# Kernel tuning notes

Hardware: AMD Instinct MI355X
Metric: run time of the kernel (lower is better)

Reference implementation:

```python
import jax, jax.numpy as jnp
import numpy as np

ALPHA = 1.5      # entmax alpha (q parameter)
N_ITER = 50      # entmax-bisect iterations (entmax library default)
B, S, DM, H, HKV, HD = 1, 2048, 2048, 16, 4, 128
ROPE_THETA = 10000.0


def _entmax_p(x):
    """alpha-entmax along last axis via bisection on tau (matches entmax.EntmaxBisect)."""
    am1 = ALPHA - 1.0
    pw = 1.0 / am1
    X = x * am1
    d = x.shape[-1]
    max_val = jnp.max(X, axis=-1, keepdims=True)
    tau_lo = max_val - 1.0                      # _gp(1, alpha) = 1
    tau_hi = max_val - (1.0 / d) ** am1          # _gp(1/d, alpha)
    dm0 = tau_hi - tau_lo

    def body(i, carry):
        tau_lo, dm, tau_m = carry
        dm = dm * 0.5
        tau_m = tau_lo + dm
        p = jnp.maximum(X - tau_m, 0.0) ** pw
        f = jnp.sum(p, axis=-1, keepdims=True) - 1.0
        tau_lo = jnp.where(f >= 0, tau_m, tau_lo)
        return (tau_lo, dm, tau_m)

    tau_lo, dm, tau_m = jax.lax.fori_loop(0, N_ITER, body, (tau_lo, dm0, tau_lo))
    p = jnp.maximum(X - tau_m, 0.0) ** pw
    return p / jnp.sum(p, axis=-1, keepdims=True)  # ensure_sum_one


@jax.custom_vjp
def entmax_bisect(x):
    return _entmax_p(x)

def _emx_fwd(x):
    p = _entmax_p(x)
    return p, p

def _emx_bwd(p, g):
    # entmax library backward: gppr = p^(2-alpha) on support
    gppr = jnp.where(p > 0, p ** (2.0 - ALPHA), 0.0)
    dX = g * gppr
    q = jnp.sum(dX, axis=-1, keepdims=True) / jnp.sum(gppr, axis=-1, keepdims=True)
    return ((dX - q * gppr),)

entmax_bisect.defvjp(_emx_fwd, _emx_bwd)


def _rotate_half(x):
    x1, x2 = x[..., : HD // 2], x[..., HD // 2:]
    return jnp.concatenate([-x2, x1], axis=-1)


def setup_inputs() -> dict:
    key = jax.random.key(0)
    k1, k2, k3, k4, k5 = jax.random.split(key, 5)
    hidden_states = jax.random.normal(k1, (B, S, DM), dtype=jnp.float32)
    wq = jax.random.normal(k2, (H * HD, DM), dtype=jnp.float32) * 0.02
    wk = jax.random.normal(k3, (HKV * HD, DM), dtype=jnp.float32) * 0.02
    wv = jax.random.normal(k4, (HKV * HD, DM), dtype=jnp.float32) * 0.02
    wo = jax.random.normal(k5, (DM, H * HD), dtype=jnp.float32) * 0.02
    # real Llama RoPE position embeddings
    inv_freq = 1.0 / (ROPE_THETA ** (np.arange(0, HD, 2, dtype=np.float32) / HD))
    pos = np.arange(S, dtype=np.float32)
    freqs = pos[:, None] * inv_freq[None, :]          # [S, HD/2]
    emb = np.concatenate([freqs, freqs], axis=-1)     # [S, HD]
    cos = jnp.asarray(np.cos(emb))[None]              # [1, S, HD]
    sin = jnp.asarray(np.sin(emb))[None]
    return {"hidden_states": hidden_states, "cos": cos, "sin": sin,
            "wq": wq, "wk": wk, "wv": wv, "wo": wo}


def reference(hidden_states, cos, sin, wq, wk, wv, wo):
    b, s, _ = hidden_states.shape
    scaling = HD ** -0.5
    # QKV projections -> [B, H, S, HD]
    q = (hidden_states @ wq.T).reshape(b, s, H, HD).transpose(0, 2, 1, 3)
    k = (hidden_states @ wk.T).reshape(b, s, HKV, HD).transpose(0, 2, 1, 3)
    v = (hidden_states @ wv.T).reshape(b, s, HKV, HD).transpose(0, 2, 1, 3)
    # RoPE (cos/sin broadcast over head axis)
    c, sn = cos[:, None, :, :], sin[:, None, :, :]
    q = q * c + _rotate_half(q) * sn
    k = k * c + _rotate_half(k) * sn
    # GQA: repeat kv heads
    g = H // HKV
    k = jnp.repeat(k, g, axis=1)
    v = jnp.repeat(v, g, axis=1)
    scores = jnp.einsum('bhqd,bhkd->bhqk', q, k) * scaling
    causal = jnp.tril(jnp.ones((s, s), dtype=bool))
    scores = jnp.where(causal, scores, -jnp.inf)
    attn = entmax_bisect(scores)                      # [B, H, S, S]
    out = jnp.einsum('bhqk,bhkd->bhqd', attn, v)
    out = out.transpose(0, 2, 1, 3).reshape(b, s, H * HD)
    out = out @ wo.T
    return (out, attn)
```

## Files before the change

### kernel.cpp

```cpp
#include <hip/hip_runtime.h>

typedef __bf16 bf16;
typedef __bf16 bf16x4 __attribute__((ext_vector_type(4)));
typedef __bf16 bf16x8 __attribute__((ext_vector_type(8)));
typedef float f32x4 __attribute__((ext_vector_type(4)));
typedef float f32x2 __attribute__((ext_vector_type(2)));

#define S 2048
#define DM 2048
#define HD 128
#define H 16
#define NQKV 3072
#define NEWTON_ITERS 12

__device__ __forceinline__ void gl2lds16(const void* g, void* l) {
    __builtin_amdgcn_global_load_lds(
        (const __attribute__((address_space(1))) void*)g,
        (__attribute__((address_space(3))) void*)l, 16, 0, 0);
}

__device__ __forceinline__ void nt_store4(f32x4 v, float* p) {
    __builtin_nontemporal_store(v, (f32x4*)p);
}

template <int CTRL, int RM>
__device__ __forceinline__ float dpp_zero(float x) {
    return __builtin_bit_cast(float, __builtin_amdgcn_update_dpp(
        0, __builtin_bit_cast(int, x), CTRL, RM, 0xf, false));
}
template <int CTRL, int RM>
__device__ __forceinline__ float dpp_self(float x) {
    int xi = __builtin_bit_cast(int, x);
    return __builtin_bit_cast(float, __builtin_amdgcn_update_dpp(xi, xi, CTRL, RM, 0xf, false));
}
__device__ __forceinline__ float wave_bcast63(float x) {
    return __builtin_bit_cast(float, __builtin_amdgcn_readlane(__builtin_bit_cast(int, x), 63));
}
__device__ __forceinline__ float wave_sum(float x) {
    x += dpp_zero<0x111, 0xf>(x);
    x += dpp_zero<0x112, 0xf>(x);
    x += dpp_zero<0x114, 0xf>(x);
    x += dpp_zero<0x118, 0xf>(x);
    x += dpp_zero<0x142, 0xa>(x);
    x += dpp_zero<0x143, 0xc>(x);
    return wave_bcast63(x);
}
__device__ __forceinline__ float wave_fmax(float x) {
    x = fmaxf(x, dpp_self<0x111, 0xf>(x));
    x = fmaxf(x, dpp_self<0x112, 0xf>(x));
    x = fmaxf(x, dpp_self<0x114, 0xf>(x));
    x = fmaxf(x, dpp_self<0x118, 0xf>(x));
    x = fmaxf(x, dpp_self<0x142, 0xa>(x));
    x = fmaxf(x, dpp_self<0x143, 0xc>(x));
    return wave_bcast63(x);
}

__global__ void cvt_all(const float* __restrict__ hid, const float* __restrict__ wq,
                        const float* __restrict__ wk, const float* __restrict__ wv,
                        const float* __restrict__ wo, bf16* __restrict__ bh,
                        bf16* __restrict__ bqkv, bf16* __restrict__ bwo) {
    int i = blockIdx.x * blockDim.x + threadIdx.x;
    const float* src;
    bf16* dst;
    int off;
    if (i < 1048576) { src = hid; dst = bh; off = i; }
    else if (i < 2097152) { src = wq; dst = bqkv; off = i - 1048576; }
    else if (i < 2359296) { src = wk; dst = bqkv + 2048 * 2048; off = i - 2097152; }
    else if (i < 2621440) { src = wv; dst = bqkv + 2048 * 2048 + 512 * 2048; off = i - 2359296; }
    else { src = wo; dst = bwo; off = i - 2621440; }
    float4 f = ((const float4*)src)[off];
    bf16x4 o;
    o[0] = (bf16)f.x; o[1] = (bf16)f.y; o[2] = (bf16)f.z; o[3] = (bf16)f.w;
    ((bf16x4*)dst)[off] = o;
}

template <int BM, int BN>
__global__ __launch_bounds__(256) void gemm_bt(const bf16* __restrict__ A,
                                               const bf16* __restrict__ B,
                                               float* __restrict__ C, int Ndim, int K) {
    __shared__ bf16 As[BM * 32];
    __shared__ bf16 Bs[BN * 32];
    int m0 = blockIdx.x * BM, n0 = blockIdx.y * BN;
    int t = threadIdx.x;
    int l = t & 63, w = t >> 6;
    int lane16 = l & 15, quad = l >> 4;

    const bf16* Abase = A + (size_t)m0 * K;
    const bf16* Bbase = B + (size_t)n0 * K;

    constexpr int MI = BM / 32, NI = BN / 32;
    int wm = (w & 1) * (BM / 2), wn = (w >> 1) * (BN / 2);
    f32x4 acc[MI][NI];
#pragma unroll
    for (int i = 0; i < MI; i++)
#pragma unroll
        for (int j = 0; j < NI; j++) acc[i][j] = (f32x4){0.f, 0.f, 0.f, 0.f};

    constexpr int AG = BM * 4;
    constexpr int BG = BN * 4;

    for (int k0 = 0; k0 < K; k0 += 32) {
#pragma unroll
        for (int it = 0; it < AG / 256; it++) {
            int c = it * 256 + t;
            gl2lds16(Abase + (size_t)(c >> 2) * K + k0 + (c & 3) * 8, &As[(c - l) * 8]);
        }
#pragma unroll
        for (int it = 0; it < BG / 256; it++) {
            int c = it * 256 + t;
            gl2lds16(Bbase + (size_t)(c >> 2) * K + k0 + (c & 3) * 8, &Bs[(c - l) * 8]);
        }
        __syncthreads();
        bf16x8 af[MI], bfr[NI];
#pragma unroll
        for (int i = 0; i < MI; i++)
            af[i] = *(const bf16x8*)&As[(wm + i * 16 + lane16) * 32 + quad * 8];
#pragma unroll
        for (int j = 0; j < NI; j++)
            bfr[j] = *(const bf16x8*)&Bs[(wn + j * 16 + lane16) * 32 + quad * 8];
#pragma unroll
        for (int i = 0; i < MI; i++)
#pragma unroll
            for (int j = 0; j < NI; j++)
                acc[i][j] = __builtin_amdgcn_mfma_f32_16x16x32_bf16(af[i], bfr[j], acc[i][j], 0, 0, 0);
        __syncthreads();
    }
#pragma unroll
    for (int i = 0; i < MI; i++)
#pragma unroll
        for (int j = 0; j < NI; j++) {
            float* cp = C + (size_t)(m0 + wm + i * 16 + quad * 4) * Ndim + n0 + wn + j * 16 + lane16;
#pragma unroll
            for (int r = 0; r < 4; r++) cp[(size_t)r * Ndim] = acc[i][j][r];
        }
}

__global__ void rope_qk(const float* __restrict__ qkv, const float* __restrict__ cosb,
                        const float* __restrict__ sinb, bf16* __restrict__ qs,
                        bf16* __restrict__ kb) {
    int col = blockIdx.x * 256 + threadIdx.x;
    int s = blockIdx.y;
    const float* row = qkv + (size_t)s * NQKV;
    float v = row[col];
    if (col < DM) {
        int h = col >> 7, d = col & 127;
        float c = cosb[s * HD + d], sn = sinb[s * HD + d];
        float other = row[(h << 7) + ((d < 64) ? (d + 64) : (d - 64))];
        float rot = (d < 64) ? -other : other;
        float o = v * c + rot * sn;
        qs[((size_t)h * S + s) * HD + d] = (bf16)(o * 0.04419417382415922f);
    } else {
        int c2 = col - DM;
        int kv = c2 >> 7, d = c2 & 127;
        float c = cosb[s * HD + d], sn = sinb[s * HD + d];
        float other = row[DM + (kv << 7) + ((d < 64) ? (d + 64) : (d - 64))];
        float rot = (d < 64) ? -other : other;
        float o = v * c + rot * sn;
        kb[((size_t)kv * S + s) * HD + d] = (bf16)o;
    }
}

__global__ __launch_bounds__(256) void vtrans(const float* __restrict__ qkv, bf16* __restrict__ vT) {
    __shared__ bf16 tile[64][66];
    int s0 = blockIdx.x * 64, y0 = blockIdx.y * 64;
    int t = threadIdx.x;
    int ty = t & 63, tr = t >> 6;
#pragma unroll
    for (int i = 0; i < 16; i++) {
        int s = tr + i * 4;
        float v = qkv[(size_t)(s0 + s) * NQKV + 2560 + y0 + ty];
        tile[s][ty] = (bf16)v;
    }
    __syncthreads();
#pragma unroll
    for (int i = 0; i < 16; i++) {
        int y = tr + i * 4;
        vT[(size_t)(y0 + y) * S + s0 + ty] = tile[ty][y];
    }
}

template <int SEGS>
__device__ __forceinline__ void attn_body(const bf16* __restrict__ qs, const bf16* __restrict__ kb,
                                          const bf16* __restrict__ vT, float* __restrict__ attn,
                                          bf16* __restrict__ o, int r0, int h,
                                          float (&buf)[16][532]) {
    constexpr int NREG2 = SEGS * 4;
    int jlen = r0 + 16;
    int l = threadIdx.x & 63;
    int w = threadIdx.x >> 6;
    int lane16 = l & 15, quad = l >> 4;

    const bf16* qrow = qs + ((size_t)h * S + (r0 + lane16)) * HD + quad * 8;
    bf16x8 afrag[4];
#pragma unroll
    for (int kc = 0; kc < 4; kc++) afrag[kc] = *(const bf16x8*)(qrow + kc * 32);

    const bf16* kbase = kb + (size_t)(h >> 2) * S * HD;
    const bf16* vbase = vT + (size_t)(h >> 2) * HD * S;
    f32x2 xr[NREG2];

#pragma unroll
    for (int sgi = 0; sgi < SEGS; sgi++) {
        int j0 = sgi * 512;
        float (*sb)[532] = buf;
#pragma unroll
        for (int tt = 0; tt < 2; tt++) {
            int t = w + tt * 16;
            int jt = j0 + t * 16;
            if (jt < jlen) {
                f32x4 acc = {0.f, 0.f, 0.f, 0.f};
                const bf16* kp = kbase + (size_t)(jt + lane16) * HD + quad * 8;
#pragma unroll
                for (int kc = 0; kc < 4; kc++) {
                    bf16x8 b = *(const bf16x8*)(kp + kc * 32);
                    acc = __builtin_amdgcn_mfma_f32_16x16x32_bf16(afrag[kc], b, acc, 0, 0, 0);
                }
                if (jt + 15 > r0) {
                    int jj = jt + lane16;
#pragma unroll
                    for (int r = 0; r < 4; r++) {
                        int rowi = quad * 4 + r;
                        float v = acc[r];
                        if (jj > r0 + rowi) v = -1e30f;
                        sb[rowi][t * 16 + lane16] = v;
                    }
                } else {
#pragma unroll
                    for (int r = 0; r < 4; r++) sb[quad * 4 + r][t * 16 + lane16] = acc[r];
                }
            }
        }
        __syncthreads();
#pragma unroll
        for (int part = 0; part < 2; part++) {
            float4 fq = *(const float4*)&sb[w][part * 256 + l * 4];
            if (sgi == SEGS - 1) {
                int jb = j0 + part * 256 + l * 4;
                xr[sgi * 4 + part * 2 + 0] =
                    (f32x2){(jb + 0 < jlen) ? fq.x : -1e30f, (jb + 1 < jlen) ? fq.y : -1e30f};
                xr[sgi * 4 + part * 2 + 1] =
                    (f32x2){(jb + 2 < jlen) ? fq.z : -1e30f, (jb + 3 < jlen) ? fq.w : -1e30f};
            } else {
                xr[sgi * 4 + part * 2 + 0] = (f32x2){fq.x, fq.y};
                xr[sgi * 4 + part * 2 + 1] = (f32x2){fq.z, fq.w};
            }
        }
        __syncthreads();
    }

    float* arow = attn + ((size_t)h * S + (r0 + w)) * S;

    {
        f32x4 z4 = {0.f, 0.f, 0.f, 0.f};
        for (int j = SEGS * 512 + l * 4; j < S; j += 256) nt_store4(z4, &arow[j]);
    }

    const f32x2 z2 = {0.f, 0.f};
    float mx = -1e30f;
#pragma unroll
    for (int c = 0; c < NREG2; c++) mx = fmaxf(mx, fmaxf(xr[c][0], xr[c][1]));
    float m = wave_fmax(mx);

    float tau = m - 1.0f;
#pragma unroll 1
    for (int it = 0; it < NEWTON_ITERS; it++) {
        f32x2 tvi = {tau, tau};
        f32x2 fa = z2, fb = z2, ga = z2, gb = z2;
#pragma unroll
        for (int c = 0; c < NREG2; c += 2) {
            f32x2 t0 = __builtin_elementwise_max(xr[c] - tvi, z2);
            fa += t0 * t0; ga += t0;
            f32x2 t1 = __builtin_elementwise_max(xr[c + 1] - tvi, z2);
            fb += t1 * t1; gb += t1;
        }
        f32x2 fv = fa + fb, gv = ga + gb;
        float f = wave_sum(fv[0] + fv[1]);
        float g = wave_sum(gv[0] + gv[1]);
        tau += (f - 1.0f) / (2.0f * g + 1e-20f);
    }

    f32x2 tv = {tau, tau};
    float inv;
    {
        f32x2 sa = z2, sbv = z2;
#pragma unroll
        for (int c = 0; c < NREG2; c += 2) {
            f32x2 t0 = __builtin_elementwise_max(xr[c] - tv, z2);
            sa += t0 * t0;
            f32x2 t1 = __builtin_elementwise_max(xr[c + 1] - tv, z2);
            sbv += t1 * t1;
        }
        f32x2 sv = sa + sbv;
        float ssum = wave_sum(sv[0] + sv[1]);
        inv = 1.0f / ssum;
    }

    int jt_o = (w & 7) * 16;
    int kh = (w >> 3) * 256;
    f32x4 acc_o = {0.f, 0.f, 0.f, 0.f};
    f32x2 inv2 = {inv, inv};

    __syncthreads();
#pragma unroll
    for (int sgi = 0; sgi < SEGS; sgi++) {
        int j0 = sgi * 512;
        bf16 (*pbf)[552] = (bf16(*)[552])(&buf[0][0]);
#pragma unroll
        for (int part = 0; part < 2; part++) {
            f32x2 ta = __builtin_elementwise_max(xr[sgi * 4 + part * 2 + 0] - tv, z2);
            f32x2 tb = __builtin_elementwise_max(xr[sgi * 4 + part * 2 + 1] - tv, z2);
            f32x2 pa = (ta * ta) * inv2;
            f32x2 pb = (tb * tb) * inv2;
            f32x4 pv = {pa[0], pa[1], pb[0], pb[1]};
            nt_store4(pv, &arow[j0 + part * 256 + l * 4]);
            bf16x4 pbv;
            pbv[0] = (bf16)pv[0]; pbv[1] = (bf16)pv[1];
            pbv[2] = (bf16)pv[2]; pbv[3] = (bf16)pv[3];
            *(bf16x4*)&pbf[w][part * 256 + l * 4] = pbv;
        }
        __syncthreads();
#pragma unroll
        for (int ks = 0; ks < 8; ks++) {
            int kk = kh + ks * 32;
            bf16x8 a = *(const bf16x8*)&pbf[lane16][kk + quad * 8];
            bf16x8 b = *(const bf16x8*)(vbase + (size_t)(jt_o + lane16) * S + j0 + kk + quad * 8);
            acc_o = __builtin_amdgcn_mfma_f32_16x16x32_bf16(a, b, acc_o, 0, 0, 0);
        }
        __syncthreads();
    }

    if (w >= 8) {
#pragma unroll
        for (int r = 0; r < 4; r++) buf[w - 8][l * 4 + r] = acc_o[r];
    }
    __syncthreads();
    if (w < 8) {
        bf16* op = o + (size_t)(r0 + quad * 4) * DM + h * HD + jt_o + lane16;
#pragma unroll
        for (int r = 0; r < 4; r++) {
            float v = acc_o[r] + buf[w][l * 4 + r];
            op[(size_t)r * DM] = (bf16)v;
        }
    }
}

__global__ __launch_bounds__(1024, 8) void attn_av_all(const bf16* __restrict__ qs,
                                                       const bf16* __restrict__ kb,
                                                       const bf16* __restrict__ vT,
                                                       float* __restrict__ attn,
                                                       bf16* __restrict__ o) {
    __shared__ float buf[16][532];
    int b = blockIdx.x;
    int h = b & 15;
    int qh = b >> 4;
    attn_body<4>(qs, kb, vT, attn, o, (96 + qh) * 16, h, buf);
    __syncthreads();
    attn_body<3>(qs, kb, vT, attn, o, (64 + qh) * 16, h, buf);
    __syncthreads();
    attn_body<2>(qs, kb, vT, attn, o, (32 + qh) * 16, h, buf);
    __syncthreads();
    attn_body<1>(qs, kb, vT, attn, o, qh * 16, h, buf);
}

extern "C" void kernel_launch(void* const* d_in, const int* in_sizes, int n_in,
                              void* d_out, int out_size, void* d_ws, size_t ws_size,
                              hipStream_t stream) {
    const float* hidden = (const float*)d_in[0];
    const float* cosb   = (const float*)d_in[1];
    const float* sinb   = (const float*)d_in[2];
    const float* wq     = (const float*)d_in[3];
    const float* wk     = (const float*)d_in[4];
    const float* wv     = (const float*)d_in[5];
    const float* wo     = (const float*)d_in[6];
    char* ws = (char*)d_ws;
    bf16*  bf_hidden = (bf16*)(ws);
    bf16*  bf_wqkv   = (bf16*)(ws + 8388608);
    bf16*  bf_wo     = (bf16*)(ws + 20971520);
    float* qkv_raw   = (float*)(ws + 29360128);
    bf16*  qsb       = (bf16*)(ws + 54525952);
    bf16*  kbb       = (bf16*)(ws + 62914560);
    bf16*  vTb       = (bf16*)(ws + 65011712);
    float* out  = (float*)d_out;
    float* attn = out + 4194304;

    cvt_all<<<dim3(14336), 256, 0, stream>>>(hidden, wq, wk, wv, wo, bf_hidden, bf_wqkv, bf_wo);

    gemm_bt<64, 128><<<dim3(32, 24), 256, 0, stream>>>(bf_hidden, bf_wqkv, qkv_raw, NQKV, DM);

    rope_qk<<<dim3(10, S), 256, 0, stream>>>(qkv_raw, cosb, sinb, qsb, kbb);
    vtrans<<<dim3(32, 8), 256, 0, stream>>>(qkv_raw, vTb);

    attn_av_all<<<dim3(512), 1024, 0, stream>>>(qsb, kbb, vTb, attn, bf_hidden);

    gemm_bt<64, 128><<<dim3(32, 16), 256, 0, stream>>>(bf_hidden, bf_wo, out, DM, DM);
}
```

Measured before the change: 588.8 us.

## Use active-set quadratic solve for entmax tau, double-buffer GEMMs and P tiles

For alpha=1.5 the threshold is replaced by a short active-set solve. Each pass takes the support count and the first and second moments, solves the quadratic in closed form, and then a few clamped Newton steps follow. This cuts the iteration count from 12 Newton steps to 3+4, each step doing a bit more work. The GEMMs move to 128x128 tiles with double-buffered LDS staging to overlap loads with MFMA. The attention P tile is ping-ponged between two LDS halves, which drops one barrier per segment. Accuracy now rests on the clamps and the convergence of the shorter iteration.

```diff
diff --git a/kernel.cpp b/kernel.cpp
--- a/kernel.cpp
+++ b/kernel.cpp
@@ -11,7 +11,9 @@
 #define HD 128
 #define H 16
 #define NQKV 3072
-#define NEWTON_ITERS 12
+#define AS_ITERS 3
+#define NW_ITERS 4
+#define BROW 556
 
 __device__ __forceinline__ void gl2lds16(const void* g, void* l) {
     __builtin_amdgcn_global_load_lds(
@@ -74,61 +76,59 @@
     ((bf16x4*)dst)[off] = o;
 }
 
-template <int BM, int BN>
-__global__ __launch_bounds__(256) void gemm_bt(const bf16* __restrict__ A,
-                                               const bf16* __restrict__ B,
-                                               float* __restrict__ C, int Ndim, int K) {
-    __shared__ bf16 As[BM * 32];
-    __shared__ bf16 Bs[BN * 32];
-    int m0 = blockIdx.x * BM, n0 = blockIdx.y * BN;
+__global__ __launch_bounds__(256) void gemm128_bt(const bf16* __restrict__ A,
+                                                  const bf16* __restrict__ B,
+                                                  float* __restrict__ C, int Ndim, int K) {
+    __shared__ bf16 As[2][128 * 32];
+    __shared__ bf16 Bs[2][128 * 32];
+    int m0 = blockIdx.x * 128, n0 = blockIdx.y * 128;
     int t = threadIdx.x;
     int l = t & 63, w = t >> 6;
     int lane16 = l & 15, quad = l >> 4;
 
+    int c0 = (w * 2) * 64 + l;
+    int c1 = c0 + 64;
     const bf16* Abase = A + (size_t)m0 * K;
     const bf16* Bbase = B + (size_t)n0 * K;
 
-    constexpr int MI = BM / 32, NI = BN / 32;
-    int wm = (w & 1) * (BM / 2), wn = (w >> 1) * (BN / 2);
-    f32x4 acc[MI][NI];
-#pragma unroll
-    for (int i = 0; i < MI; i++)
-#pragma unroll
-        for (int j = 0; j < NI; j++) acc[i][j] = (f32x4){0.f, 0.f, 0.f, 0.f};
-
-    constexpr int AG = BM * 4;
-    constexpr int BG = BN * 4;
-
+    int wm = (w & 1) * 64, wn = (w >> 1) * 64;
+    f32x4 acc[4][4];
+#pragma unroll
+    for (int i = 0; i < 4; i++)
+#pragma unroll
+        for (int j = 0; j < 4; j++) acc[i][j] = (f32x4){0.f, 0.f, 0.f, 0.f};
+
+    auto stage = [&](int sel, int k0) {
+        gl2lds16(Abase + (size_t)(c0 >> 2) * K + k0 + (c0 & 3) * 8, &As[sel][(w * 2) * 512]);
+        gl2lds16(Abase + (size_t)(c1 >> 2) * K + k0 + (c1 & 3) * 8, &As[sel][(w * 2 + 1) * 512]);
+        gl2lds16(Bbase + (size_t)(c0 >> 2) * K + k0 + (c0 & 3) * 8, &Bs[sel][(w * 2) * 512]);
+        gl2lds16(Bbase + (size_t)(c1 >> 2) * K + k0 + (c1 & 3) * 8, &Bs[sel][(w * 2 + 1) * 512]);
+    };
+
+    stage(0, 0);
+    __syncthreads();
+    int cur = 0;
     for (int k0 = 0; k0 < K; k0 += 32) {
-#pragma unroll
-        for (int it = 0; it < AG / 256; it++) {
-            int c = it * 256 + t;
-            gl2lds16(Abase + (size_t)(c >> 2) * K + k0 + (c & 3) * 8, &As[(c - l) * 8]);
-        }
-#pragma unroll
-        for (int it = 0; it < BG / 256; it++) {
-            int c = it * 256 + t;
-            gl2lds16(Bbase + (size_t)(c >> 2) * K + k0 + (c & 3) * 8, &Bs[(c - l) * 8]);
-        }
-        __syncthreads();
-        bf16x8 af[MI], bfr[NI];
-#pragma unroll
-        for (int i = 0; i < MI; i++)
-            af[i] = *(const bf16x8*)&As[(wm + i * 16 + lane16) * 32 + quad * 8];
-#pragma unroll
-        for (int j = 0; j < NI; j++)
-            bfr[j] = *(const bf16x8*)&Bs[(wn + j * 16 + lane16) * 32 + quad * 8];
-#pragma unroll
-        for (int i = 0; i < MI; i++)
-#pragma unroll
-            for (int j = 0; j < NI; j++)
+        if (k0 + 32 < K) stage(cur ^ 1, k0 + 32);
+        bf16x8 af[4], bfr[4];
+#pragma unroll
+        for (int i = 0; i < 4; i++)
+            af[i] = *(const bf16x8*)&As[cur][(wm + i * 16 + lane16) * 32 + quad * 8];
+#pragma unroll
+        for (int j = 0; j < 4; j++)
+            bfr[j] = *(const bf16x8*)&Bs[cur][(wn + j * 16 + lane16) * 32 + quad * 8];
+#pragma unroll
+        for (int i = 0; i < 4; i++)
+#pragma unroll
+            for (int j = 0; j < 4; j++)
                 acc[i][j] = __builtin_amdgcn_mfma_f32_16x16x32_bf16(af[i], bfr[j], acc[i][j], 0, 0, 0);
         __syncthreads();
-    }
-#pragma unroll
-    for (int i = 0; i < MI; i++)
-#pragma unroll
-        for (int j = 0; j < NI; j++) {
+        cur ^= 1;
+    }
+#pragma unroll
+    for (int i = 0; i < 4; i++)
+#pragma unroll
+        for (int j = 0; j < 4; j++) {
             float* cp = C + (size_t)(m0 + wm + i * 16 + quad * 4) * Ndim + n0 + wn + j * 16 + lane16;
 #pragma unroll
             for (int r = 0; r < 4; r++) cp[(size_t)r * Ndim] = acc[i][j][r];
@@ -183,7 +183,7 @@
 __device__ __forceinline__ void attn_body(const bf16* __restrict__ qs, const bf16* __restrict__ kb,
                                           const bf16* __restrict__ vT, float* __restrict__ attn,
                                           bf16* __restrict__ o, int r0, int h,
-                                          float (&buf)[16][532]) {
+                                          float (&buf)[16][BROW]) {
     constexpr int NREG2 = SEGS * 4;
     int jlen = r0 + 16;
     int l = threadIdx.x & 63;
@@ -202,7 +202,6 @@
 #pragma unroll
     for (int sgi = 0; sgi < SEGS; sgi++) {
         int j0 = sgi * 512;
-        float (*sb)[532] = buf;
 #pragma unroll
         for (int tt = 0; tt < 2; tt++) {
             int t = w + tt * 16;
@@ -222,18 +221,18 @@
                         int rowi = quad * 4 + r;
                         float v = acc[r];
                         if (jj > r0 + rowi) v = -1e30f;
-                        sb[rowi][t * 16 + lane16] = v;
+                        buf[rowi][t * 16 + lane16] = v;
                     }
                 } else {
 #pragma unroll
-                    for (int r = 0; r < 4; r++) sb[quad * 4 + r][t * 16 + lane16] = acc[r];
+                    for (int r = 0; r < 4; r++) buf[quad * 4 + r][t * 16 + lane16] = acc[r];
                 }
             }
         }
         __syncthreads();
 #pragma unroll
         for (int part = 0; part < 2; part++) {
-            float4 fq = *(const float4*)&sb[w][part * 256 + l * 4];
+            float4 fq = *(const float4*)&buf[w][part * 256 + l * 4];
             if (sgi == SEGS - 1) {
                 int jb = j0 + part * 256 + l * 4;
                 xr[sgi * 4 + part * 2 + 0] =
@@ -260,10 +259,33 @@
 #pragma unroll
     for (int c = 0; c < NREG2; c++) mx = fmaxf(mx, fmaxf(xr[c][0], xr[c][1]));
     float m = wave_fmax(mx);
-
-    float tau = m - 1.0f;
+    float taulo = m - 1.0f;
+    float tauhi = m - 0.02209709f;
+    float tau = taulo;
+
 #pragma unroll 1
-    for (int it = 0; it < NEWTON_ITERS; it++) {
+    for (int it = 0; it < AS_ITERS; it++) {
+        f32x2 tvi = {tau, tau};
+        f32x2 b1a = z2, b1b = z2, b2a = z2, b2b = z2, cna = z2, cnb = z2;
+#pragma unroll
+        for (int c = 0; c < NREG2; c += 2) {
+            f32x2 t0 = __builtin_elementwise_max(xr[c] - tvi, z2);
+            b2a += t0 * t0; b1a += t0;
+            cna += (f32x2){t0[0] > 0.f ? 1.f : 0.f, t0[1] > 0.f ? 1.f : 0.f};
+            f32x2 t1 = __builtin_elementwise_max(xr[c + 1] - tvi, z2);
+            b2b += t1 * t1; b1b += t1;
+            cnb += (f32x2){t1[0] > 0.f ? 1.f : 0.f, t1[1] > 0.f ? 1.f : 0.f};
+        }
+        f32x2 s1 = b1a + b1b, s2 = b2a + b2b, sc = cna + cnb;
+        float B1 = wave_sum(s1[0] + s1[1]);
+        float B2 = wave_sum(s2[0] + s2[1]);
+        float n = wave_sum(sc[0] + sc[1]);
+        float disc = fmaxf(B1 * B1 - n * (B2 - 1.0f), 0.f);
+        tau += (B1 - __builtin_sqrtf(disc)) / fmaxf(n, 1.0f);
+        tau = fminf(fmaxf(tau, taulo), tauhi);
+    }
+#pragma unroll 1
+    for (int it = 0; it < NW_ITERS; it++) {
         f32x2 tvi = {tau, tau};
         f32x2 fa = z2, fb = z2, ga = z2, gb = z2;
 #pragma unroll
@@ -277,6 +299,7 @@
         float f = wave_sum(fv[0] + fv[1]);
         float g = wave_sum(gv[0] + gv[1]);
         tau += (f - 1.0f) / (2.0f * g + 1e-20f);
+        tau = fminf(fmaxf(tau, taulo), tauhi);
     }
 
     f32x2 tv = {tau, tau};
@@ -300,35 +323,34 @@
     f32x4 acc_o = {0.f, 0.f, 0.f, 0.f};
     f32x2 inv2 = {inv, inv};
 
-    __syncthreads();
 #pragma unroll
     for (int sgi = 0; sgi < SEGS; sgi++) {
         int j0 = sgi * 512;
-        bf16 (*pbf)[552] = (bf16(*)[552])(&buf[0][0]);
+        bf16 (*pb)[BROW] = (bf16(*)[BROW])(&buf[0][0]) + (sgi & 1) * 16;
 #pragma unroll
         for (int part = 0; part < 2; part++) {
             f32x2 ta = __builtin_elementwise_max(xr[sgi * 4 + part * 2 + 0] - tv, z2);
             f32x2 tb = __builtin_elementwise_max(xr[sgi * 4 + part * 2 + 1] - tv, z2);
             f32x2 pa = (ta * ta) * inv2;
-            f32x2 pb = (tb * tb) * inv2;
-            f32x4 pv = {pa[0], pa[1], pb[0], pb[1]};
+            f32x2 pb2 = (tb * tb) * inv2;
+            f32x4 pv = {pa[0], pa[1], pb2[0], pb2[1]};
             nt_store4(pv, &arow[j0 + part * 256 + l * 4]);
             bf16x4 pbv;
             pbv[0] = (bf16)pv[0]; pbv[1] = (bf16)pv[1];
             pbv[2] = (bf16)pv[2]; pbv[3] = (bf16)pv[3];
-            *(bf16x4*)&pbf[w][part * 256 + l * 4] = pbv;
+            *(bf16x4*)&pb[w][part * 256 + l * 4] = pbv;
         }
         __syncthreads();
 #pragma unroll
         for (int ks = 0; ks < 8; ks++) {
             int kk = kh + ks * 32;
-            bf16x8 a = *(const bf16x8*)&pbf[lane16][kk + quad * 8];
+            bf16x8 a = *(const bf16x8*)&pb[lane16][kk + quad * 8];
             bf16x8 b = *(const bf16x8*)(vbase + (size_t)(jt_o + lane16) * S + j0 + kk + quad * 8);
             acc_o = __builtin_amdgcn_mfma_f32_16x16x32_bf16(a, b, acc_o, 0, 0, 0);
         }
-        __syncthreads();
-    }
-
+    }
+
+    __syncthreads();
     if (w >= 8) {
 #pragma unroll
         for (int r = 0; r < 4; r++) buf[w - 8][l * 4 + r] = acc_o[r];
@@ -349,7 +371,7 @@
                                                        const bf16* __restrict__ vT,
                                                        float* __restrict__ attn,
                                                        bf16* __restrict__ o) {
-    __shared__ float buf[16][532];
+    __shared__ float buf[16][BROW];
     int b = blockIdx.x;
     int h = b & 15;
     int qh = b >> 4;
@@ -385,12 +407,12 @@
 
     cvt_all<<<dim3(14336), 256, 0, stream>>>(hidden, wq, wk, wv, wo, bf_hidden, bf_wqkv, bf_wo);
 
-    gemm_bt<64, 128><<<dim3(32, 24), 256, 0, stream>>>(bf_hidden, bf_wqkv, qkv_raw, NQKV, DM);
+    gemm128_bt<<<dim3(16, 24), 256, 0, stream>>>(bf_hidden, bf_wqkv, qkv_raw, NQKV, DM);
 
     rope_qk<<<dim3(10, S), 256, 0, stream>>>(qkv_raw, cosb, sinb, qsb, kbb);
     vtrans<<<dim3(32, 8), 256, 0, stream>>>(qkv_raw, vTb);
 
     attn_av_all<<<dim3(512), 1024, 0, stream>>>(qsb, kbb, vTb, attn, bf_hidden);
 
-    gemm_bt<64, 128><<<dim3(32, 16), 256, 0, stream>>>(bf_hidden, bf_wo, out, DM, DM);
-}
+    gemm128_bt<<<dim3(16, 16), 256, 0, stream>>>(bf_hidden, bf_wo, out, DM, DM);
+}
```

Result: no change. 586.8 us (-0.3%).
